# Kernel optimization log

Hardware: AMD Instinct MI355X
Metric: run time of the kernel (lower is better)

Reference implementation:

```python
import jax, jax.numpy as jnp
import numpy as np

BATCH = 4096
INSTANCES = 8
NUM_CLASSES = 512
D_FEAT = 128
MARGIN_N = 2.5
MARGIN_P = 2.0
TEMP = 10.0
NEG_INF = -1e30


def _masks(B, instances):
    # pos_mask[i,j] = (i//instances == j//instances) & strict-upper-triangle
    lab = jnp.arange(B) // instances
    same = lab[:, None] == lab[None, :]
    tri = jnp.triu(jnp.ones((B, B), dtype=bool), 1)
    return same & tri, tri & ~same  # pos_mask, neg_mask


def _masked_exp_loss(dist, mask, margin, temp, fallback):
    # original: w_ij = exp(temp*(margin_ij - dist_ij)) on masked entries,
    # loss = -(w/sum(w) * dist).sum(). Max-shift is mathematically invariant.
    logit = jnp.where(mask, temp * (margin - dist), NEG_INF)
    m = jax.lax.stop_gradient(jnp.max(logit))
    w = jnp.where(mask, jnp.exp(logit - m), 0.0)
    sw = w.sum()
    loss = -(w * dist).sum() / jnp.where(sw > 0, sw, 1.0)
    return jnp.where(mask.any(), loss, jnp.float32(fallback))


def setup_inputs() -> dict:
    key = jax.random.key(0)
    k1, k2, k3, k4, k5 = jax.random.split(key, 5)
    x = 0.1 * jax.random.normal(k1, (BATCH, D_FEAT), dtype=jnp.float32)
    y = jax.random.randint(k2, (BATCH,), 0, NUM_CLASSES)
    # mean shifted so the adaptive-margin bands overlap dist (~2*D*0.01=2.56)
    mean = jax.random.normal(k3, (NUM_CLASSES, NUM_CLASSES), dtype=jnp.float32) + 2.5
    std = jax.random.uniform(k4, (NUM_CLASSES, NUM_CLASSES), dtype=jnp.float32)
    noise = jax.random.normal(k5, (BATCH, BATCH), dtype=jnp.float32)
    return {"x": x, "y": y, "mean": mean, "std": std, "noise": noise}


def reference(x, y, mean, std, noise):
    B = x.shape[0]
    pos_mask, neg_mask = _masks(B, INSTANCES)

    cls_mean = mean[y][:, y]              # [B, B]
    cls_std = std[y][:, y]                # [B, B]
    cls_obs = cls_mean + cls_std * noise  # torch.normal(cls_mean, cls_std)

    sq = jnp.sum(x * x, axis=1)
    dist = -2.0 * (x @ x.T) + sq[None, :] + sq[:, None]  # [B, B]

    thr_n1 = cls_obs - MARGIN_N * cls_std
    thr_mid = cls_obs - (MARGIN_N - 1.0) * cls_std
    thr_hi = cls_obs + (MARGIN_N - 1.0) * cls_std
    thr_p = cls_obs + MARGIN_P * cls_std

    loss_n1 = _masked_exp_loss(dist, (dist < thr_n1) & neg_mask, thr_n1, TEMP, -0.0001)
    loss_n2 = _masked_exp_loss(
        dist, (dist > thr_n1) & (dist < thr_mid) & neg_mask, thr_mid, TEMP - 5.0, -0.0001)
    loss_n3 = _masked_exp_loss(
        dist, (dist > thr_mid) & (dist < thr_hi) & neg_mask, thr_hi, TEMP - 5.0, -0.0001)

    mask_p = (dist > thr_p) & pos_mask
    filt = jnp.where(mask_p, dist, 0.0)
    s = filt.sum()
    loss_p1 = jnp.where(
        mask_p.any(), (filt * filt).sum() / jnp.where(s != 0, s, 1.0), jnp.float32(0.0001))

    loss = 1.0 + (loss_n1 + loss_n2 + loss_n3 + loss_p1) / 4.0
    return dist, loss
```

## Files before the change

kernel.cpp:

```cpp
#include <hip/hip_runtime.h>
#include <hip/hip_bf16.h>

#define B 4096
#define DFEAT 128
#define NCLS 512
#define NEG_INF_F (-1e30f)

typedef __attribute__((ext_vector_type(8))) short bf16x8;
typedef __attribute__((ext_vector_type(4))) float f32x4;

__device__ __forceinline__ unsigned short f2bf(float f) {
    unsigned int u = __float_as_uint(f);
    unsigned int r = (u + 0x7fffu + ((u >> 16) & 1u)) >> 16;
    return (unsigned short)r;
}

__device__ __forceinline__ void oupd(float logit, float d, float& m, float& sw, float& swd) {
    if (logit > m) {
        float e = __expf(m - logit);
        sw  = fmaf(sw, e, 1.0f);
        swd = fmaf(swd, e, d);
        m = logit;
    } else {
        float e = __expf(logit - m);
        sw += e;
        swd = fmaf(e, d, swd);
    }
}

__device__ __forceinline__ void omerge(float& m, float& sw, float& swd,
                                       float m2, float sw2, float swd2) {
    float M = fmaxf(m, m2);
    float e1 = __expf(m - M);
    float e2 = __expf(m2 - M);
    sw  = sw * e1 + sw2 * e2;
    swd = swd * e1 + swd2 * e2;
    m = M;
}

__device__ __forceinline__ void neg_update(float d, float mu, float sg, float nz, float st[12]) {
    float obs = fmaf(sg, nz, mu);
    float t1 = fmaf(-2.5f, sg, obs);
    if (d < t1) {
        oupd(10.0f * (t1 - d), d, st[0], st[1], st[2]);
    } else {
        float tm = fmaf(-1.5f, sg, obs);
        if (d < tm) {
            if (d > t1) oupd(5.0f * (tm - d), d, st[3], st[4], st[5]);
        } else {
            float th = fmaf(1.5f, sg, obs);
            if (d < th && d > tm) oupd(5.0f * (th - d), d, st[6], st[7], st[8]);
        }
    }
}

__device__ __forceinline__ void wave_reduce12(float st[12]) {
    #pragma unroll
    for (int off = 32; off; off >>= 1) {
        float o[12];
        #pragma unroll
        for (int k = 0; k < 12; ++k) o[k] = __shfl_down(st[k], off);
        omerge(st[0], st[1], st[2], o[0], o[1], o[2]);
        omerge(st[3], st[4], st[5], o[3], o[4], o[5]);
        omerge(st[6], st[7], st[8], o[6], o[7], o[8]);
        st[9] += o[9]; st[10] += o[10]; st[11] += o[11];
    }
}

__global__ void prep_kernel(const float* __restrict__ x,
                            unsigned int* __restrict__ xbf_packed,
                            float* __restrict__ sq) {
    int row = blockIdx.x;
    int lane = threadIdx.x;
    float2 v = ((const float2*)(x + row * DFEAT))[lane];
    float ss = fmaf(v.x, v.x, v.y * v.y);
    unsigned int pk = ((unsigned int)f2bf(v.y) << 16) | (unsigned int)f2bf(v.x);
    xbf_packed[row * (DFEAT / 2) + lane] = pk;
    #pragma unroll
    for (int off = 32; off; off >>= 1) ss += __shfl_down(ss, off);
    if (lane == 0) sq[row] = ss;
}

__launch_bounds__(256)
__global__ void dist_kernel(const unsigned short* __restrict__ xbf,
                            const float* __restrict__ sq,
                            float* __restrict__ out) {
    const int bx = blockIdx.x;
    const int by = blockIdx.y;
    const int tid = threadIdx.x;
    const int wave = tid >> 6;
    const int lane = tid & 63;
    const int q = lane >> 4;
    const int l16 = lane & 15;
    const int row0 = by * 128 + (wave >> 1) * 64;
    const int col0 = bx * 128 + (wave & 1) * 64;

    f32x4 acc[4][4];
    #pragma unroll
    for (int r = 0; r < 4; ++r)
        #pragma unroll
        for (int c = 0; c < 4; ++c)
            acc[r][c] = (f32x4){0.f, 0.f, 0.f, 0.f};

    #pragma unroll
    for (int kk = 0; kk < 4; ++kk) {
        const int ko = kk * 32 + q * 8;
        bf16x8 afr[4], bfr[4];
        #pragma unroll
        for (int r = 0; r < 4; ++r)
            afr[r] = *(const bf16x8*)(xbf + (row0 + r * 16 + l16) * DFEAT + ko);
        #pragma unroll
        for (int c = 0; c < 4; ++c)
            bfr[c] = *(const bf16x8*)(xbf + (col0 + c * 16 + l16) * DFEAT + ko);
        #pragma unroll
        for (int r = 0; r < 4; ++r)
            #pragma unroll
            for (int c = 0; c < 4; ++c)
                acc[r][c] = __builtin_amdgcn_mfma_f32_16x16x32_bf16(afr[r], bfr[c], acc[r][c], 0, 0, 0);
    }

    float sqr[4][4];
    #pragma unroll
    for (int r = 0; r < 4; ++r)
        *(f32x4*)sqr[r] = *(const f32x4*)(sq + row0 + r * 16 + q * 4);
    int cols[4]; float sqc[4];
    #pragma unroll
    for (int c = 0; c < 4; ++c) {
        cols[c] = col0 + c * 16 + l16;
        sqc[c] = sq[cols[c]];
    }

    #pragma unroll
    for (int r = 0; r < 4; ++r) {
        #pragma unroll
        for (int t = 0; t < 4; ++t) {
            int base = (row0 + r * 16 + q * 4 + t) * B;
            float s = sqr[r][t];
            #pragma unroll
            for (int c = 0; c < 4; ++c)
                out[base + cols[c]] = fmaf(-2.0f, acc[r][c][t], s + sqc[c]);
        }
    }
}

__device__ __forceinline__ void process_row(int row,
                                            const float* __restrict__ drow,
                                            const float* __restrict__ nrow,
                                            const int* __restrict__ y,
                                            const float* __restrict__ muS,
                                            const float* __restrict__ sgS,
                                            int tid, float st[12]) {
    const int ge = row | 7;
    const int npos = ge - row;
    if (tid < npos) {
        int col = row + 1 + tid;
        float d = drow[col], nz = nrow[col];
        int yc = y[col];
        float sg = sgS[yc];
        float obs = fmaf(sg, nz, muS[yc]);
        float tp = fmaf(2.0f, sg, obs);
        if (d > tp) { st[9] += d; st[10] = fmaf(d, d, st[10]); st[11] += 1.0f; }
    }
    for (int col = ge + 1 + tid * 4; col < B; col += 1024) {
        float4 d4 = *(const float4*)(drow + col);
        float4 n4 = *(const float4*)(nrow + col);
        int4  y4 = *(const int4*)(y + col);
        neg_update(d4.x, muS[y4.x], sgS[y4.x], n4.x, st);
        neg_update(d4.y, muS[y4.y], sgS[y4.y], n4.y, st);
        neg_update(d4.z, muS[y4.z], sgS[y4.z], n4.z, st);
        neg_update(d4.w, muS[y4.w], sgS[y4.w], n4.w, st);
    }
}

__launch_bounds__(256)
__global__ void loss_kernel(const float* __restrict__ dist,
                            const float* __restrict__ noise,
                            const int* __restrict__ y,
                            const float* __restrict__ meant,
                            const float* __restrict__ stdt,
                            float* __restrict__ partials) {
    const int b = blockIdx.x;
    const int i = b;
    const int j = B - 1 - b;
    const int tid = threadIdx.x;
    const int lane = tid & 63, wave = tid >> 6;

    __shared__ float mu0[NCLS], sg0[NCLS], mu1[NCLS], sg1[NCLS];
    const int yi = y[i], yj = y[j];
    for (int c = tid * 4; c < NCLS; c += 1024) {
        *(float4*)(mu0 + c) = *(const float4*)(meant + yi * NCLS + c);
        *(float4*)(sg0 + c) = *(const float4*)(stdt  + yi * NCLS + c);
        *(float4*)(mu1 + c) = *(const float4*)(meant + yj * NCLS + c);
        *(float4*)(sg1 + c) = *(const float4*)(stdt  + yj * NCLS + c);
    }
    __syncthreads();

    float st[12];
    st[0] = st[3] = st[6] = NEG_INF_F;
    st[1] = st[2] = st[4] = st[5] = st[7] = st[8] = st[9] = st[10] = st[11] = 0.f;

    process_row(i, dist + (size_t)i * B, noise + (size_t)i * B, y, mu0, sg0, tid, st);
    process_row(j, dist + (size_t)j * B, noise + (size_t)j * B, y, mu1, sg1, tid, st);

    wave_reduce12(st);

    __shared__ float red[4][12];
    if (lane == 0) {
        #pragma unroll
        for (int k = 0; k < 12; ++k) red[wave][k] = st[k];
    }
    __syncthreads();
    if (tid == 0) {
        float r0[12];
        #pragma unroll
        for (int k = 0; k < 12; ++k) r0[k] = red[0][k];
        #pragma unroll
        for (int w = 1; w < 4; ++w) {
            omerge(r0[0], r0[1], r0[2], red[w][0], red[w][1], red[w][2]);
            omerge(r0[3], r0[4], r0[5], red[w][3], red[w][4], red[w][5]);
            omerge(r0[6], r0[7], r0[8], red[w][6], red[w][7], red[w][8]);
            r0[9] += red[w][9]; r0[10] += red[w][10]; r0[11] += red[w][11];
        }
        float* pp = partials + b * 12;
        #pragma unroll
        for (int k = 0; k < 12; ++k) pp[k] = r0[k];
    }
}

__global__ void finalize_kernel(const float* __restrict__ partials,
                                float* __restrict__ out) {
    int tid = threadIdx.x;
    int lane = tid & 63, wave = tid >> 6;
    float st[12];
    st[0] = st[3] = st[6] = NEG_INF_F;
    st[1] = st[2] = st[4] = st[5] = st[7] = st[8] = st[9] = st[10] = st[11] = 0.f;
    for (int p = tid; p < 2048; p += 256) {
        const float* pp = partials + p * 12;
        omerge(st[0], st[1], st[2], pp[0], pp[1], pp[2]);
        omerge(st[3], st[4], st[5], pp[3], pp[4], pp[5]);
        omerge(st[6], st[7], st[8], pp[6], pp[7], pp[8]);
        st[9] += pp[9]; st[10] += pp[10]; st[11] += pp[11];
    }
    wave_reduce12(st);
    __shared__ float red[4][12];
    if (lane == 0) {
        #pragma unroll
        for (int k = 0; k < 12; ++k) red[wave][k] = st[k];
    }
    __syncthreads();
    if (tid == 0) {
        float r0[12];
        #pragma unroll
        for (int k = 0; k < 12; ++k) r0[k] = red[0][k];
        #pragma unroll
        for (int w = 1; w < 4; ++w) {
            omerge(r0[0], r0[1], r0[2], red[w][0], red[w][1], red[w][2]);
            omerge(r0[3], r0[4], r0[5], red[w][3], red[w][4], red[w][5]);
            omerge(r0[6], r0[7], r0[8], red[w][6], red[w][7], red[w][8]);
            r0[9] += red[w][9]; r0[10] += red[w][10]; r0[11] += red[w][11];
        }
        float ln1 = (r0[1] > 0.f) ? -(r0[2] / r0[1]) : -0.0001f;
        float ln2 = (r0[4] > 0.f) ? -(r0[5] / r0[4]) : -0.0001f;
        float ln3 = (r0[7] > 0.f) ? -(r0[8] / r0[7]) : -0.0001f;
        float lp  = (r0[11] > 0.f) ? (r0[10] / ((r0[9] != 0.f) ? r0[9] : 1.f)) : 0.0001f;
        out[(size_t)B * B] = 1.0f + 0.25f * (ln1 + ln2 + ln3 + lp);
    }
}

extern "C" void kernel_launch(void* const* d_in, const int* in_sizes, int n_in,
                              void* d_out, int out_size, void* d_ws, size_t ws_size,
                              hipStream_t stream) {
    const float* x     = (const float*)d_in[0];
    const int*   y     = (const int*)d_in[1];
    const float* meant = (const float*)d_in[2];
    const float* stdt  = (const float*)d_in[3];
    const float* noise = (const float*)d_in[4];
    float* out = (float*)d_out;
    char* ws = (char*)d_ws;
    unsigned short* xbf = (unsigned short*)ws;
    float* sq           = (float*)(ws + 1048576);
    float* partials     = (float*)(ws + 1064960);

    hipLaunchKernelGGL(prep_kernel, dim3(B), dim3(64), 0, stream,
                       x, (unsigned int*)xbf, sq);
    hipLaunchKernelGGL(dist_kernel, dim3(32, 32), dim3(256), 0, stream,
                       xbf, sq, out);
    hipLaunchKernelGGL(loss_kernel, dim3(2048), dim3(256), 0, stream,
                       out, noise, y, meant, stdt, partials);
    hipLaunchKernelGGL(finalize_kernel, dim3(1), dim3(256), 0, stream,
                       partials, out);
}
```

Baseline: 161.5 us.

## Fuse distance GEMM with loss computation in one kernel

Merges the distance kernel and the loss kernel, so each 128x128 tile computes its distances and accumulates loss statistics straight from registers. Tiles below the diagonal only write distances plus neutral partials. This removes the second kernel's re-read of the 64MB dist matrix and one launch. In exchange, mean/std are gathered directly from global memory with scattered per-element indexing instead of staged shared-memory rows, and the noise reads become strided per row, which may hurt coalescing and load balance across tiles.

```diff
diff --git a/kernel.cpp b/kernel.cpp
--- a/kernel.cpp
+++ b/kernel.cpp
@@ -82,9 +82,14 @@
 }
 
 __launch_bounds__(256)
-__global__ void dist_kernel(const unsigned short* __restrict__ xbf,
-                            const float* __restrict__ sq,
-                            float* __restrict__ out) {
+__global__ void fused_kernel(const unsigned short* __restrict__ xbf,
+                             const float* __restrict__ sq,
+                             const float* __restrict__ noise,
+                             const int* __restrict__ y,
+                             const float* __restrict__ meant,
+                             const float* __restrict__ stdt,
+                             float* __restrict__ out,
+                             float* __restrict__ partials) {
     const int bx = blockIdx.x;
     const int by = blockIdx.y;
     const int tid = threadIdx.x;
@@ -94,6 +99,7 @@
     const int l16 = lane & 15;
     const int row0 = by * 128 + (wave >> 1) * 64;
     const int col0 = bx * 128 + (wave & 1) * 64;
+    const int blin = by * 32 + bx;
 
     f32x4 acc[4][4];
     #pragma unroll
@@ -130,77 +136,56 @@
         sqc[c] = sq[cols[c]];
     }
 
-    #pragma unroll
-    for (int r = 0; r < 4; ++r) {
-        #pragma unroll
-        for (int t = 0; t < 4; ++t) {
-            int base = (row0 + r * 16 + q * 4 + t) * B;
-            float s = sqr[r][t];
-            #pragma unroll
-            for (int c = 0; c < 4; ++c)
-                out[base + cols[c]] = fmaf(-2.0f, acc[r][c][t], s + sqc[c]);
-        }
-    }
-}
-
-__device__ __forceinline__ void process_row(int row,
-                                            const float* __restrict__ drow,
-                                            const float* __restrict__ nrow,
-                                            const int* __restrict__ y,
-                                            const float* __restrict__ muS,
-                                            const float* __restrict__ sgS,
-                                            int tid, float st[12]) {
-    const int ge = row | 7;
-    const int npos = ge - row;
-    if (tid < npos) {
-        int col = row + 1 + tid;
-        float d = drow[col], nz = nrow[col];
-        int yc = y[col];
-        float sg = sgS[yc];
-        float obs = fmaf(sg, nz, muS[yc]);
-        float tp = fmaf(2.0f, sg, obs);
-        if (d > tp) { st[9] += d; st[10] = fmaf(d, d, st[10]); st[11] += 1.0f; }
-    }
-    for (int col = ge + 1 + tid * 4; col < B; col += 1024) {
-        float4 d4 = *(const float4*)(drow + col);
-        float4 n4 = *(const float4*)(nrow + col);
-        int4  y4 = *(const int4*)(y + col);
-        neg_update(d4.x, muS[y4.x], sgS[y4.x], n4.x, st);
-        neg_update(d4.y, muS[y4.y], sgS[y4.y], n4.y, st);
-        neg_update(d4.z, muS[y4.z], sgS[y4.z], n4.z, st);
-        neg_update(d4.w, muS[y4.w], sgS[y4.w], n4.w, st);
-    }
-}
-
-__launch_bounds__(256)
-__global__ void loss_kernel(const float* __restrict__ dist,
-                            const float* __restrict__ noise,
-                            const int* __restrict__ y,
-                            const float* __restrict__ meant,
-                            const float* __restrict__ stdt,
-                            float* __restrict__ partials) {
-    const int b = blockIdx.x;
-    const int i = b;
-    const int j = B - 1 - b;
-    const int tid = threadIdx.x;
-    const int lane = tid & 63, wave = tid >> 6;
-
-    __shared__ float mu0[NCLS], sg0[NCLS], mu1[NCLS], sg1[NCLS];
-    const int yi = y[i], yj = y[j];
-    for (int c = tid * 4; c < NCLS; c += 1024) {
-        *(float4*)(mu0 + c) = *(const float4*)(meant + yi * NCLS + c);
-        *(float4*)(sg0 + c) = *(const float4*)(stdt  + yi * NCLS + c);
-        *(float4*)(mu1 + c) = *(const float4*)(meant + yj * NCLS + c);
-        *(float4*)(sg1 + c) = *(const float4*)(stdt  + yj * NCLS + c);
-    }
-    __syncthreads();
+    const bool doLoss = (bx >= by);
+    const bool diag   = (bx == by);
+
+    int yj[4];
+    #pragma unroll
+    for (int c = 0; c < 4; ++c) yj[c] = doLoss ? y[cols[c]] : 0;
 
     float st[12];
     st[0] = st[3] = st[6] = NEG_INF_F;
     st[1] = st[2] = st[4] = st[5] = st[7] = st[8] = st[9] = st[10] = st[11] = 0.f;
 
-    process_row(i, dist + (size_t)i * B, noise + (size_t)i * B, y, mu0, sg0, tid, st);
-    process_row(j, dist + (size_t)j * B, noise + (size_t)j * B, y, mu1, sg1, tid, st);
+    #pragma unroll
+    for (int r = 0; r < 4; ++r) {
+        #pragma unroll
+        for (int t = 0; t < 4; ++t) {
+            const int i = row0 + r * 16 + q * 4 + t;
+            const size_t base = (size_t)i * B;
+            const float si = sqr[r][t];
+            const int yi = doLoss ? y[i] : 0;
+            #pragma unroll
+            for (int c = 0; c < 4; ++c) {
+                const int j = cols[c];
+                const float d = fmaf(-2.0f, acc[r][c][t], si + sqc[c]);
+                out[base + j] = d;
+                if (doLoss && (!diag || j > i)) {
+                    const int idx = yi * NCLS + yj[c];
+                    const float mu = meant[idx];
+                    const float sg = stdt[idx];
+                    const float nz = noise[base + j];
+                    if (diag && (((i ^ j) >> 3) == 0)) {
+                        const float obs = fmaf(sg, nz, mu);
+                        const float tp = fmaf(2.0f, sg, obs);
+                        if (d > tp) { st[9] += d; st[10] = fmaf(d, d, st[10]); st[11] += 1.0f; }
+                    } else {
+                        neg_update(d, mu, sg, nz, st);
+                    }
+                }
+            }
+        }
+    }
+
+    if (!doLoss) {
+        if (tid == 0) {
+            float* pp = partials + blin * 12;
+            pp[0] = pp[3] = pp[6] = NEG_INF_F;
+            pp[1] = pp[2] = pp[4] = pp[5] = 0.f;
+            pp[7] = pp[8] = pp[9] = pp[10] = pp[11] = 0.f;
+        }
+        return;
+    }
 
     wave_reduce12(st);
 
@@ -221,7 +206,7 @@
             omerge(r0[6], r0[7], r0[8], red[w][6], red[w][7], red[w][8]);
             r0[9] += red[w][9]; r0[10] += red[w][10]; r0[11] += red[w][11];
         }
-        float* pp = partials + b * 12;
+        float* pp = partials + blin * 12;
         #pragma unroll
         for (int k = 0; k < 12; ++k) pp[k] = r0[k];
     }
@@ -234,7 +219,7 @@
     float st[12];
     st[0] = st[3] = st[6] = NEG_INF_F;
     st[1] = st[2] = st[4] = st[5] = st[7] = st[8] = st[9] = st[10] = st[11] = 0.f;
-    for (int p = tid; p < 2048; p += 256) {
+    for (int p = tid; p < 1024; p += 256) {
         const float* pp = partials + p * 12;
         omerge(st[0], st[1], st[2], pp[0], pp[1], pp[2]);
         omerge(st[3], st[4], st[5], pp[3], pp[4], pp[5]);
@@ -283,10 +268,8 @@
 
     hipLaunchKernelGGL(prep_kernel, dim3(B), dim3(64), 0, stream,
                        x, (unsigned int*)xbf, sq);
-    hipLaunchKernelGGL(dist_kernel, dim3(32, 32), dim3(256), 0, stream,
-                       xbf, sq, out);
-    hipLaunchKernelGGL(loss_kernel, dim3(2048), dim3(256), 0, stream,
-                       out, noise, y, meant, stdt, partials);
+    hipLaunchKernelGGL(fused_kernel, dim3(32, 32), dim3(256), 0, stream,
+                       xbf, sq, noise, y, meant, stdt, out, partials);
     hipLaunchKernelGGL(finalize_kernel, dim3(1), dim3(256), 0, stream,
                        partials, out);
 }
```

Result: slower. 262.6 us (+62.6%).
